# Kernel tuning notes

Measured on AMD Instinct MI355X. Metric: run time of the kernel, lower is better.

## Reference

```python
import jax, jax.numpy as jnp
import numpy as np

EPS = 1e-05
IN_FEATURES = 1024
OUT_FEATURES = 512
M = 65536


def setup_inputs() -> dict:
    key = jax.random.key(0)
    k_x, k_w, k_b = jax.random.split(key, 3)
    x = jax.random.normal(k_x, (M, IN_FEATURES), dtype=jnp.float32)
    # kaiming_uniform(a=sqrt(5)) on [out, in]: bound = sqrt(6/((1+a^2)*fan_in)) = 1/sqrt(fan_in)
    bound = 1.0 / np.sqrt(IN_FEATURES)
    weight = jax.random.uniform(k_w, (OUT_FEATURES, IN_FEATURES), dtype=jnp.float32,
                                minval=-bound, maxval=bound)
    bias = jax.random.uniform(k_b, (OUT_FEATURES,), dtype=jnp.float32,
                              minval=-bound, maxval=bound)
    gamma = jnp.ones((OUT_FEATURES,), dtype=jnp.float32)
    beta = jnp.zeros((OUT_FEATURES,), dtype=jnp.float32)
    scale = jnp.ones((1,), dtype=jnp.float32)
    return {"x": x, "weight": weight, "bias": bias,
            "gamma": gamma, "beta": beta, "scale": scale}


def reference(x, weight, bias, gamma, beta, scale):
    # GEMM + bias: [M, N]
    acc = jnp.einsum('mk,nk->mn', x, weight) + bias[None, :]
    # Row-wise normalization over N (as the fused kernel computes per row)
    mean = jnp.mean(acc, axis=1, keepdims=True)
    var = jnp.mean((acc - mean) ** 2, axis=1, keepdims=True)
    normalized = (acc - mean) / jnp.sqrt(var + EPS)
    scaled = (normalized * gamma[None, :] + beta[None, :]) * scale[0]
    # Row softmax over N
    return jax.nn.softmax(scaled, axis=1)
```

## Files before the change

kernel.cpp:

```cpp
#include <hip/hip_runtime.h>
#include <hip/hip_bf16.h>

constexpr int KD = 1024;
constexpr int ND = 512;
constexpr int NT = 16;
constexpr float EPSV = 1e-5f;

using f32x4  = __attribute__((ext_vector_type(4))) float;
using bf16x8 = __attribute__((ext_vector_type(8))) short;
using u16x8  = __attribute__((ext_vector_type(8))) unsigned short;

__device__ __forceinline__ unsigned short f2bf(float f) {
  unsigned int u = __builtin_bit_cast(unsigned int, f);
  return (unsigned short)((u + 0x7fffu + ((u >> 16) & 1u)) >> 16);
}

__device__ __forceinline__ u16x8 pack8(float4 a, float4 b) {
  u16x8 v;
  v[0] = f2bf(a.x); v[1] = f2bf(a.y); v[2] = f2bf(a.z); v[3] = f2bf(a.w);
  v[4] = f2bf(b.x); v[5] = f2bf(b.y); v[6] = f2bf(b.z); v[7] = f2bf(b.w);
  return v;
}

__device__ __forceinline__ unsigned short cvt1(float f) {
  __hip_bfloat16 h = __float2bfloat16(f);
  return __builtin_bit_cast(unsigned short, h);
}

__device__ __forceinline__ void gload16(const void* g, void* l) {
  __builtin_amdgcn_global_load_lds(
      (const __attribute__((address_space(1))) void*)g,
      (__attribute__((address_space(3))) void*)l, 16, 0, 0);
}

#define WAITV8()  asm volatile("s_waitcnt vmcnt(8)" ::: "memory")
#define WAITV0()  asm volatile("s_waitcnt vmcnt(0)" ::: "memory")
#define LGKM0()   do { asm volatile("s_waitcnt lgkmcnt(0)" ::: "memory"); \
                       __builtin_amdgcn_sched_barrier(0); } while (0)
#define SCHEDB()  __builtin_amdgcn_sched_barrier(0)

__global__ void wconvert_kernel(const float* __restrict__ w,
                                unsigned short* __restrict__ wb) {
  int i = (blockIdx.x * blockDim.x + threadIdx.x) * 8;
  float4 a = *reinterpret_cast<const float4*>(w + i);
  float4 b = *reinterpret_cast<const float4*>(w + i + 4);
  *reinterpret_cast<u16x8*>(wb + i) = pack8(a, b);
}

__global__ __launch_bounds__(512, 2)
void fused_kernel(const float* __restrict__ x,
                  const unsigned short* __restrict__ wb,
                  const float* __restrict__ bias,
                  const float* __restrict__ gamma,
                  const float* __restrict__ beta,
                  const float* __restrict__ scalep,
                  float* __restrict__ out) {
  __shared__ unsigned short As[128 * 64];
  __shared__ unsigned short Bs[2][512 * 64];

  const int tid  = threadIdx.x;
  const int lane = tid & 63;
  const int wid  = tid >> 6;
  const int wr   = wid >> 2;
  const int wcq  = wid & 3;
  const int l15  = lane & 15;
  const int lg   = lane >> 4;

  const long bm  = (long)blockIdx.x * 128;

  f32x4 acc[4][8] = {};

  const int arow0 = wid * 16 + lg;
  const float* asrc = x + (bm + arow0) * KD + l15 * 4;
  int aw[4];
  #pragma unroll
  for (int q = 0; q < 4; ++q) {
    int row = arow0 + q * 4;
    aw[q] = row * 128 + (((l15 >> 1) ^ (row & 7)) * 16) + ((l15 & 1) * 8);
  }

  int bsrc[8];
  #pragma unroll
  for (int p = 0; p < 8; ++p) {
    int n = p * 64 + (tid >> 3);
    int u = (tid & 7) ^ (n & 7);
    bsrc[p] = n * KD + u * 8;
  }

  int ard[4], brd[8];
  #pragma unroll
  for (int i = 0; i < 4; ++i) {
    int row = wr * 64 + i * 16 + l15;
    ard[i] = row * 128 + (lg ^ (row & 7)) * 16;
  }
  #pragma unroll
  for (int i = 0; i < 8; ++i) {
    int n = wcq * 128 + i * 16 + l15;
    brd[i] = n * 128 + (lg ^ (n & 7)) * 16;
  }

#define ISSUE_A(t) do { \
    qa0 = *reinterpret_cast<const float4*>(asrc + (t) * 64 + 0 * 4 * KD); \
    qa1 = *reinterpret_cast<const float4*>(asrc + (t) * 64 + 1 * 4 * KD); \
    qa2 = *reinterpret_cast<const float4*>(asrc + (t) * 64 + 2 * 4 * KD); \
    qa3 = *reinterpret_cast<const float4*>(asrc + (t) * 64 + 3 * 4 * KD); } while (0)

#define ISSUE_B(t, bufi) do { \
    gload16(wb + bsrc[0] + (t) * 64, (char*)Bs[bufi] + 0 * 8192 + tid * 16); \
    gload16(wb + bsrc[1] + (t) * 64, (char*)Bs[bufi] + 1 * 8192 + tid * 16); \
    gload16(wb + bsrc[2] + (t) * 64, (char*)Bs[bufi] + 2 * 8192 + tid * 16); \
    gload16(wb + bsrc[3] + (t) * 64, (char*)Bs[bufi] + 3 * 8192 + tid * 16); \
    gload16(wb + bsrc[4] + (t) * 64, (char*)Bs[bufi] + 4 * 8192 + tid * 16); \
    gload16(wb + bsrc[5] + (t) * 64, (char*)Bs[bufi] + 5 * 8192 + tid * 16); \
    gload16(wb + bsrc[6] + (t) * 64, (char*)Bs[bufi] + 6 * 8192 + tid * 16); \
    gload16(wb + bsrc[7] + (t) * 64, (char*)Bs[bufi] + 7 * 8192 + tid * 16); } while (0)

#define WA1(qr, qi) do { \
    union { unsigned short s[4]; unsigned long long v; } c_; \
    c_.s[0] = cvt1(qr.x); c_.s[1] = cvt1(qr.y); \
    c_.s[2] = cvt1(qr.z); c_.s[3] = cvt1(qr.w); \
    *reinterpret_cast<unsigned long long*>((char*)As + aw[qi]) = c_.v; } while (0)

#define WRITE_A() do { WA1(qa0, 0); WA1(qa1, 1); WA1(qa2, 2); WA1(qa3, 3); } while (0)

#define COMPUTE(bufi) do { \
    const char* ab_ = (const char*)As; \
    const char* bb_ = (const char*)Bs[bufi]; \
    _Pragma("unroll") \
    for (int ks = 0; ks < 2; ++ks) { \
      const int kx_ = ks * 64; \
      bf16x8 b0_ = *reinterpret_cast<const bf16x8*>(bb_ + (brd[0] ^ kx_)); \
      bf16x8 b1_ = *reinterpret_cast<const bf16x8*>(bb_ + (brd[1] ^ kx_)); \
      bf16x8 b2_ = *reinterpret_cast<const bf16x8*>(bb_ + (brd[2] ^ kx_)); \
      bf16x8 b3_ = *reinterpret_cast<const bf16x8*>(bb_ + (brd[3] ^ kx_)); \
      bf16x8 b4_ = *reinterpret_cast<const bf16x8*>(bb_ + (brd[4] ^ kx_)); \
      bf16x8 b5_ = *reinterpret_cast<const bf16x8*>(bb_ + (brd[5] ^ kx_)); \
      bf16x8 b6_ = *reinterpret_cast<const bf16x8*>(bb_ + (brd[6] ^ kx_)); \
      bf16x8 b7_ = *reinterpret_cast<const bf16x8*>(bb_ + (brd[7] ^ kx_)); \
      _Pragma("unroll") \
      for (int mi = 0; mi < 4; ++mi) { \
        bf16x8 af_ = *reinterpret_cast<const bf16x8*>(ab_ + (ard[mi] ^ kx_)); \
        acc[mi][0] = __builtin_amdgcn_mfma_f32_16x16x32_bf16(af_, b0_, acc[mi][0], 0, 0, 0); \
        acc[mi][1] = __builtin_amdgcn_mfma_f32_16x16x32_bf16(af_, b1_, acc[mi][1], 0, 0, 0); \
        acc[mi][2] = __builtin_amdgcn_mfma_f32_16x16x32_bf16(af_, b2_, acc[mi][2], 0, 0, 0); \
        acc[mi][3] = __builtin_amdgcn_mfma_f32_16x16x32_bf16(af_, b3_, acc[mi][3], 0, 0, 0); \
        acc[mi][4] = __builtin_amdgcn_mfma_f32_16x16x32_bf16(af_, b4_, acc[mi][4], 0, 0, 0); \
        acc[mi][5] = __builtin_amdgcn_mfma_f32_16x16x32_bf16(af_, b5_, acc[mi][5], 0, 0, 0); \
        acc[mi][6] = __builtin_amdgcn_mfma_f32_16x16x32_bf16(af_, b6_, acc[mi][6], 0, 0, 0); \
        acc[mi][7] = __builtin_amdgcn_mfma_f32_16x16x32_bf16(af_, b7_, acc[mi][7], 0, 0, 0); \
      } \
    } } while (0)

  float4 qa0, qa1, qa2, qa3;

  ISSUE_A(0);    SCHEDB();
  ISSUE_B(0, 0); SCHEDB();
  WAITV8();
  WRITE_A();
  WAITV0();
  LGKM0();
  __builtin_amdgcn_s_barrier();
  SCHEDB();

  for (int t = 0; t < NT; ++t) {
    const int cur = t & 1;
    const int tp  = (t + 1 < NT) ? t + 1 : NT - 1;
    ISSUE_A(tp);          SCHEDB();
    ISSUE_B(tp, cur ^ 1); SCHEDB();
    COMPUTE(cur);
    SCHEDB();
    __builtin_amdgcn_s_barrier();
    SCHEDB();
    WAITV8();
    WRITE_A();
    WAITV0();
    LGKM0();
    __builtin_amdgcn_s_barrier();
    SCHEDB();
  }

  float* redS = (float*)As;
  float* redQ = redS + 640;
  float* rowA = redQ + 640;
  float* rowB = rowA + 128;

  const int col0 = wcq * 128 + l15;
  const float sc = scalep[0];
  float bs8[8], gs8[8], bb8[8];
  #pragma unroll
  for (int ni = 0; ni < 8; ++ni) {
    bs8[ni] = bias[col0 + ni * 16];
    gs8[ni] = gamma[col0 + ni * 16] * sc;
    bb8[ni] = beta[col0 + ni * 16] * sc;
  }

  #pragma unroll
  for (int mi = 0; mi < 4; ++mi) {
    #pragma unroll
    for (int j = 0; j < 4; ++j) {
      float s = 0.f, q = 0.f;
      #pragma unroll
      for (int ni = 0; ni < 8; ++ni) {
        float v = acc[mi][ni][j] + bs8[ni];
        acc[mi][ni][j] = v;
        s += v;
        q = fmaf(v, v, q);
      }
      #pragma unroll
      for (int m = 1; m < 16; m <<= 1) {
        s += __shfl_xor(s, m, 64);
        q += __shfl_xor(q, m, 64);
      }
      if (l15 == 0) {
        int r = wr * 64 + mi * 16 + lg * 4 + j;
        redS[r * 5 + wcq] = s;
        redQ[r * 5 + wcq] = q;
      }
    }
  }
  __syncthreads();
  if (tid < 128) {
    float s = redS[tid * 5 + 0] + redS[tid * 5 + 1] + redS[tid * 5 + 2] + redS[tid * 5 + 3];
    float q = redQ[tid * 5 + 0] + redQ[tid * 5 + 1] + redQ[tid * 5 + 2] + redQ[tid * 5 + 3];
    float mu = s * (1.f / ND);
    rowA[tid] = mu;
    rowB[tid] = rsqrtf(q * (1.f / ND) - mu * mu + EPSV);
  }
  __syncthreads();

  #pragma unroll
  for (int mi = 0; mi < 4; ++mi) {
    #pragma unroll
    for (int j = 0; j < 4; ++j) {
      int r = wr * 64 + mi * 16 + lg * 4 + j;
      float mu = rowA[r], rs = rowB[r];
      float pm = -3.402823466e38f;
      #pragma unroll
      for (int ni = 0; ni < 8; ++ni) {
        float v = (acc[mi][ni][j] - mu) * rs;
        v = fmaf(v, gs8[ni], bb8[ni]);
        acc[mi][ni][j] = v;
        pm = fmaxf(pm, v);
      }
      #pragma unroll
      for (int m = 1; m < 16; m <<= 1) pm = fmaxf(pm, __shfl_xor(pm, m, 64));
      if (l15 == 0) redS[r * 5 + wcq] = pm;
    }
  }
  __syncthreads();
  if (tid < 128) {
    rowA[tid] = fmaxf(fmaxf(redS[tid * 5 + 0], redS[tid * 5 + 1]),
                      fmaxf(redS[tid * 5 + 2], redS[tid * 5 + 3]));
  }
  __syncthreads();

  #pragma unroll
  for (int mi = 0; mi < 4; ++mi) {
    #pragma unroll
    for (int j = 0; j < 4; ++j) {
      int r = wr * 64 + mi * 16 + lg * 4 + j;
      float rmx = rowA[r];
      float ps = 0.f;
      #pragma unroll
      for (int ni = 0; ni < 8; ++ni) {
        float e = __expf(acc[mi][ni][j] - rmx);
        acc[mi][ni][j] = e;
        ps += e;
      }
      #pragma unroll
      for (int m = 1; m < 16; m <<= 1) ps += __shfl_xor(ps, m, 64);
      if (l15 == 0) redQ[r * 5 + wcq] = ps;
    }
  }
  __syncthreads();
  if (tid < 128) {
    rowB[tid] = 1.f / (redQ[tid * 5 + 0] + redQ[tid * 5 + 1] +
                       redQ[tid * 5 + 2] + redQ[tid * 5 + 3]);
  }
  __syncthreads();

  #pragma unroll
  for (int mi = 0; mi < 4; ++mi) {
    #pragma unroll
    for (int j = 0; j < 4; ++j) {
      int r = wr * 64 + mi * 16 + lg * 4 + j;
      float rd = rowB[r];
      float* op = out + (bm + r) * ND + col0;
      #pragma unroll
      for (int ni = 0; ni < 8; ++ni)
        __builtin_nontemporal_store(acc[mi][ni][j] * rd, op + ni * 16);
    }
  }
#undef ISSUE_A
#undef ISSUE_B
#undef WA1
#undef WRITE_A
#undef COMPUTE
}

__global__ void fused_fallback(const float* __restrict__ x,
                               const float* __restrict__ wf,
                               const float* __restrict__ bias,
                               const float* __restrict__ gamma,
                               const float* __restrict__ beta,
                               const float* __restrict__ scalep,
                               float* __restrict__ out) {
  long row = blockIdx.x;
  int t = threadIdx.x;
  float s = 0.f;
  const float* xr = x + row * KD;
  const float* wr_ = wf + (size_t)t * KD;
  for (int k = 0; k < KD; ++k) s += xr[k] * wr_[k];
  s += bias[t];
  __shared__ float buf[ND];
  buf[t] = s;
  __syncthreads();
  __shared__ float red[2];
  if (t == 0) {
    float sum = 0.f, sq = 0.f;
    for (int i = 0; i < ND; ++i) { sum += buf[i]; sq += buf[i] * buf[i]; }
    float mu = sum / ND;
    red[0] = mu;
    red[1] = rsqrtf(sq / ND - mu * mu + EPSV);
  }
  __syncthreads();
  float zv = (s - red[0]) * red[1] * gamma[t] * scalep[0] + beta[t] * scalep[0];
  buf[t] = zv;
  __syncthreads();
  __shared__ float red2[2];
  if (t == 0) {
    float mxv = -3.4e38f;
    for (int i = 0; i < ND; ++i) mxv = fmaxf(mxv, buf[i]);
    float den = 0.f;
    for (int i = 0; i < ND; ++i) den += __expf(buf[i] - mxv);
    red2[0] = mxv; red2[1] = 1.f / den;
  }
  __syncthreads();
  out[row * ND + t] = __expf(zv - red2[0]) * red2[1];
}

extern "C" void kernel_launch(void* const* d_in, const int* in_sizes, int n_in,
                              void* d_out, int out_size, void* d_ws, size_t ws_size,
                              hipStream_t stream) {
  const float* x     = (const float*)d_in[0];
  const float* w     = (const float*)d_in[1];
  const float* bias  = (const float*)d_in[2];
  const float* gamma = (const float*)d_in[3];
  const float* beta  = (const float*)d_in[4];
  const float* scale = (const float*)d_in[5];
  float* out = (float*)d_out;

  const int Mrows = in_sizes[0] / KD;
  const size_t wb_bytes = (size_t)ND * KD * sizeof(unsigned short);

  if (ws_size >= wb_bytes) {
    unsigned short* wbuf = (unsigned short*)d_ws;
    wconvert_kernel<<<(ND * KD) / (256 * 8), 256, 0, stream>>>(w, wbuf);
    fused_kernel<<<Mrows / 128, 512, 0, stream>>>(x, wbuf, bias, gamma, beta,
                                                  scale, out);
  } else {
    fused_fallback<<<Mrows, ND, 0, stream>>>(x, w, bias, gamma, beta, scale, out);
  }
}
```

Before: 142.9 us.

## Double-buffer A tile in LDS and split compute into two prioritized phases

Adds a second shared-memory buffer for the converted x tile, so the next tile's A writes go to the other buffer and the mid-iteration barrier can be dropped. The compute step is split into two k-phases, and the B prefetch is issued between them so its global-to-LDS loads overlap the first phase. Each phase loads its fragments, waits on lgkmcnt, and raises wave priority around the MFMA block. LDS use grows by 16 KB per block, which could threaten the two-blocks-per-CU occupancy target.

Result: no change. 140.5 us (-1.7%).

```diff
diff --git a/kernel.cpp b/kernel.cpp
--- a/kernel.cpp
+++ b/kernel.cpp
@@ -25,6 +25,11 @@
 __device__ __forceinline__ unsigned short cvt1(float f) {
   __hip_bfloat16 h = __float2bfloat16(f);
   return __builtin_bit_cast(unsigned short, h);
+}
+
+__device__ __forceinline__ float bf2f(unsigned short s) {
+  unsigned int u = (unsigned int)s << 16;
+  return __builtin_bit_cast(float, u);
 }
 
 __device__ __forceinline__ void gload16(const void* g, void* l) {
@@ -55,7 +60,7 @@
                   const float* __restrict__ beta,
                   const float* __restrict__ scalep,
                   float* __restrict__ out) {
-  __shared__ unsigned short As[128 * 64];
+  __shared__ unsigned short As[2][128 * 64];
   __shared__ unsigned short Bs[2][512 * 64];
 
   const int tid  = threadIdx.x;
@@ -115,48 +120,74 @@
     gload16(wb + bsrc[6] + (t) * 64, (char*)Bs[bufi] + 6 * 8192 + tid * 16); \
     gload16(wb + bsrc[7] + (t) * 64, (char*)Bs[bufi] + 7 * 8192 + tid * 16); } while (0)
 
-#define WA1(qr, qi) do { \
+#define WA1(qr, qi, bufi) do { \
     union { unsigned short s[4]; unsigned long long v; } c_; \
     c_.s[0] = cvt1(qr.x); c_.s[1] = cvt1(qr.y); \
     c_.s[2] = cvt1(qr.z); c_.s[3] = cvt1(qr.w); \
-    *reinterpret_cast<unsigned long long*>((char*)As + aw[qi]) = c_.v; } while (0)
-
-#define WRITE_A() do { WA1(qa0, 0); WA1(qa1, 1); WA1(qa2, 2); WA1(qa3, 3); } while (0)
-
-#define COMPUTE(bufi) do { \
-    const char* ab_ = (const char*)As; \
-    const char* bb_ = (const char*)Bs[bufi]; \
-    _Pragma("unroll") \
-    for (int ks = 0; ks < 2; ++ks) { \
-      const int kx_ = ks * 64; \
-      bf16x8 b0_ = *reinterpret_cast<const bf16x8*>(bb_ + (brd[0] ^ kx_)); \
-      bf16x8 b1_ = *reinterpret_cast<const bf16x8*>(bb_ + (brd[1] ^ kx_)); \
-      bf16x8 b2_ = *reinterpret_cast<const bf16x8*>(bb_ + (brd[2] ^ kx_)); \
-      bf16x8 b3_ = *reinterpret_cast<const bf16x8*>(bb_ + (brd[3] ^ kx_)); \
-      bf16x8 b4_ = *reinterpret_cast<const bf16x8*>(bb_ + (brd[4] ^ kx_)); \
-      bf16x8 b5_ = *reinterpret_cast<const bf16x8*>(bb_ + (brd[5] ^ kx_)); \
-      bf16x8 b6_ = *reinterpret_cast<const bf16x8*>(bb_ + (brd[6] ^ kx_)); \
-      bf16x8 b7_ = *reinterpret_cast<const bf16x8*>(bb_ + (brd[7] ^ kx_)); \
-      _Pragma("unroll") \
-      for (int mi = 0; mi < 4; ++mi) { \
-        bf16x8 af_ = *reinterpret_cast<const bf16x8*>(ab_ + (ard[mi] ^ kx_)); \
-        acc[mi][0] = __builtin_amdgcn_mfma_f32_16x16x32_bf16(af_, b0_, acc[mi][0], 0, 0, 0); \
-        acc[mi][1] = __builtin_amdgcn_mfma_f32_16x16x32_bf16(af_, b1_, acc[mi][1], 0, 0, 0); \
-        acc[mi][2] = __builtin_amdgcn_mfma_f32_16x16x32_bf16(af_, b2_, acc[mi][2], 0, 0, 0); \
-        acc[mi][3] = __builtin_amdgcn_mfma_f32_16x16x32_bf16(af_, b3_, acc[mi][3], 0, 0, 0); \
-        acc[mi][4] = __builtin_amdgcn_mfma_f32_16x16x32_bf16(af_, b4_, acc[mi][4], 0, 0, 0); \
-        acc[mi][5] = __builtin_amdgcn_mfma_f32_16x16x32_bf16(af_, b5_, acc[mi][5], 0, 0, 0); \
-        acc[mi][6] = __builtin_amdgcn_mfma_f32_16x16x32_bf16(af_, b6_, acc[mi][6], 0, 0, 0); \
-        acc[mi][7] = __builtin_amdgcn_mfma_f32_16x16x32_bf16(af_, b7_, acc[mi][7], 0, 0, 0); \
-      } \
-    } } while (0)
+    *reinterpret_cast<unsigned long long*>((char*)As[bufi] + aw[qi]) = c_.v; } while (0)
+
+#define WRITE_A(bufi) do { const int wb_ = (bufi); \
+    WA1(qa0, 0, wb_); WA1(qa1, 1, wb_); WA1(qa2, 2, wb_); WA1(qa3, 3, wb_); } while (0)
+
+#define PHASE(ks, bufc) do { \
+    const char* ab_ = (const char*)As[bufc]; \
+    const char* bb_ = (const char*)Bs[bufc]; \
+    const int kx_ = (ks) * 64; \
+    bf16x8 b0_ = *reinterpret_cast<const bf16x8*>(bb_ + (brd[0] ^ kx_)); \
+    bf16x8 b1_ = *reinterpret_cast<const bf16x8*>(bb_ + (brd[1] ^ kx_)); \
+    bf16x8 b2_ = *reinterpret_cast<const bf16x8*>(bb_ + (brd[2] ^ kx_)); \
+    bf16x8 b3_ = *reinterpret_cast<const bf16x8*>(bb_ + (brd[3] ^ kx_)); \
+    bf16x8 b4_ = *reinterpret_cast<const bf16x8*>(bb_ + (brd[4] ^ kx_)); \
+    bf16x8 b5_ = *reinterpret_cast<const bf16x8*>(bb_ + (brd[5] ^ kx_)); \
+    bf16x8 b6_ = *reinterpret_cast<const bf16x8*>(bb_ + (brd[6] ^ kx_)); \
+    bf16x8 b7_ = *reinterpret_cast<const bf16x8*>(bb_ + (brd[7] ^ kx_)); \
+    bf16x8 a0_ = *reinterpret_cast<const bf16x8*>(ab_ + (ard[0] ^ kx_)); \
+    bf16x8 a1_ = *reinterpret_cast<const bf16x8*>(ab_ + (ard[1] ^ kx_)); \
+    bf16x8 a2_ = *reinterpret_cast<const bf16x8*>(ab_ + (ard[2] ^ kx_)); \
+    bf16x8 a3_ = *reinterpret_cast<const bf16x8*>(ab_ + (ard[3] ^ kx_)); \
+    LGKM0(); \
+    __builtin_amdgcn_s_setprio(1); \
+    acc[0][0] = __builtin_amdgcn_mfma_f32_16x16x32_bf16(a0_, b0_, acc[0][0], 0, 0, 0); \
+    acc[0][1] = __builtin_amdgcn_mfma_f32_16x16x32_bf16(a0_, b1_, acc[0][1], 0, 0, 0); \
+    acc[0][2] = __builtin_amdgcn_mfma_f32_16x16x32_bf16(a0_, b2_, acc[0][2], 0, 0, 0); \
+    acc[0][3] = __builtin_amdgcn_mfma_f32_16x16x32_bf16(a0_, b3_, acc[0][3], 0, 0, 0); \
+    acc[0][4] = __builtin_amdgcn_mfma_f32_16x16x32_bf16(a0_, b4_, acc[0][4], 0, 0, 0); \
+    acc[0][5] = __builtin_amdgcn_mfma_f32_16x16x32_bf16(a0_, b5_, acc[0][5], 0, 0, 0); \
+    acc[0][6] = __builtin_amdgcn_mfma_f32_16x16x32_bf16(a0_, b6_, acc[0][6], 0, 0, 0); \
+    acc[0][7] = __builtin_amdgcn_mfma_f32_16x16x32_bf16(a0_, b7_, acc[0][7], 0, 0, 0); \
+    acc[1][0] = __builtin_amdgcn_mfma_f32_16x16x32_bf16(a1_, b0_, acc[1][0], 0, 0, 0); \
+    acc[1][1] = __builtin_amdgcn_mfma_f32_16x16x32_bf16(a1_, b1_, acc[1][1], 0, 0, 0); \
+    acc[1][2] = __builtin_amdgcn_mfma_f32_16x16x32_bf16(a1_, b2_, acc[1][2], 0, 0, 0); \
+    acc[1][3] = __builtin_amdgcn_mfma_f32_16x16x32_bf16(a1_, b3_, acc[1][3], 0, 0, 0); \
+    acc[1][4] = __builtin_amdgcn_mfma_f32_16x16x32_bf16(a1_, b4_, acc[1][4], 0, 0, 0); \
+    acc[1][5] = __builtin_amdgcn_mfma_f32_16x16x32_bf16(a1_, b5_, acc[1][5], 0, 0, 0); \
+    acc[1][6] = __builtin_amdgcn_mfma_f32_16x16x32_bf16(a1_, b6_, acc[1][6], 0, 0, 0); \
+    acc[1][7] = __builtin_amdgcn_mfma_f32_16x16x32_bf16(a1_, b7_, acc[1][7], 0, 0, 0); \
+    acc[2][0] = __builtin_amdgcn_mfma_f32_16x16x32_bf16(a2_, b0_, acc[2][0], 0, 0, 0); \
+    acc[2][1] = __builtin_amdgcn_mfma_f32_16x16x32_bf16(a2_, b1_, acc[2][1], 0, 0, 0); \
+    acc[2][2] = __builtin_amdgcn_mfma_f32_16x16x32_bf16(a2_, b2_, acc[2][2], 0, 0, 0); \
+    acc[2][3] = __builtin_amdgcn_mfma_f32_16x16x32_bf16(a2_, b3_, acc[2][3], 0, 0, 0); \
+    acc[2][4] = __builtin_amdgcn_mfma_f32_16x16x32_bf16(a2_, b4_, acc[2][4], 0, 0, 0); \
+    acc[2][5] = __builtin_amdgcn_mfma_f32_16x16x32_bf16(a2_, b5_, acc[2][5], 0, 0, 0); \
+    acc[2][6] = __builtin_amdgcn_mfma_f32_16x16x32_bf16(a2_, b6_, acc[2][6], 0, 0, 0); \
+    acc[2][7] = __builtin_amdgcn_mfma_f32_16x16x32_bf16(a2_, b7_, acc[2][7], 0, 0, 0); \
+    acc[3][0] = __builtin_amdgcn_mfma_f32_16x16x32_bf16(a3_, b0_, acc[3][0], 0, 0, 0); \
+    acc[3][1] = __builtin_amdgcn_mfma_f32_16x16x32_bf16(a3_, b1_, acc[3][1], 0, 0, 0); \
+    acc[3][2] = __builtin_amdgcn_mfma_f32_16x16x32_bf16(a3_, b2_, acc[3][2], 0, 0, 0); \
+    acc[3][3] = __builtin_amdgcn_mfma_f32_16x16x32_bf16(a3_, b3_, acc[3][3], 0, 0, 0); \
+    acc[3][4] = __builtin_amdgcn_mfma_f32_16x16x32_bf16(a3_, b4_, acc[3][4], 0, 0, 0); \
+    acc[3][5] = __builtin_amdgcn_mfma_f32_16x16x32_bf16(a3_, b5_, acc[3][5], 0, 0, 0); \
+    acc[3][6] = __builtin_amdgcn_mfma_f32_16x16x32_bf16(a3_, b6_, acc[3][6], 0, 0, 0); \
+    acc[3][7] = __builtin_amdgcn_mfma_f32_16x16x32_bf16(a3_, b7_, acc[3][7], 0, 0, 0); \
+    __builtin_amdgcn_s_setprio(0); \
+    SCHEDB(); } while (0)
 
   float4 qa0, qa1, qa2, qa3;
 
   ISSUE_A(0);    SCHEDB();
   ISSUE_B(0, 0); SCHEDB();
   WAITV8();
-  WRITE_A();
+  WRITE_A(0);
   WAITV0();
   LGKM0();
   __builtin_amdgcn_s_barrier();
@@ -166,20 +197,18 @@
     const int cur = t & 1;
     const int tp  = (t + 1 < NT) ? t + 1 : NT - 1;
     ISSUE_A(tp);          SCHEDB();
+    PHASE(0, cur);
     ISSUE_B(tp, cur ^ 1); SCHEDB();
-    COMPUTE(cur);
-    SCHEDB();
-    __builtin_amdgcn_s_barrier();
-    SCHEDB();
+    PHASE(1, cur);
     WAITV8();
-    WRITE_A();
+    WRITE_A(cur ^ 1);
     WAITV0();
     LGKM0();
     __builtin_amdgcn_s_barrier();
     SCHEDB();
   }
 
-  float* redS = (float*)As;
+  float* redS = (float*)As[0];
   float* redQ = redS + 640;
   float* rowA = redQ + 640;
   float* rowB = rowA + 128;
@@ -295,7 +324,7 @@
 #undef ISSUE_B
 #undef WA1
 #undef WRITE_A
-#undef COMPUTE
+#undef PHASE
 }
 
 __global__ void fused_fallback(const float* __restrict__ x,
```
